# Kernel tuning notes

Hardware: AMD Instinct MI355X
Metric: run time of the kernel (lower is better)

## Reference

```python
import jax, jax.numpy as jnp
import numpy as np

BN_EPS = 1e-5


def _weight_mlp(off, Wh, bh, Wo, bo):
    # off: [Nout, k, 2] relative neighbor offsets -> [Nout, k, 9] interp coeffs
    h = jax.nn.relu(off @ Wh + bh)
    return h @ Wo + bo


def _interp_conv(x, idx, off, Wk, bk, Wh, bh, Wo, bo):
    # x: [B, Cin, Nin]; idx: [Nout, k] neighbor indices into Nin; Wk: [Cout, Cin, 9]
    a = _weight_mlp(off, Wh, bh, Wo, bo)        # [Nout, k, 9]
    feats = x[:, :, idx]                         # gather -> [B, Cin, Nout, k]
    # dynamic filter: per-neighbor kernel = a @ Wk taps, contracted with features
    y = jnp.einsum('nkt,bcnk,oct->bon', a, feats, Wk)  # [B, Cout, Nout]
    return y + bk[None, :, None]


def _bn_relu(x, g, b):
    # BatchNorm1d over [B, C, N] using batch statistics (training-mode forward)
    mean = x.mean(axis=(0, 2), keepdims=True)
    var = x.var(axis=(0, 2), keepdims=True)
    xn = (x - mean) * jax.lax.rsqrt(var + BN_EPS)
    return jax.nn.relu(xn * g[None, :, None] + b[None, :, None])


def setup_inputs() -> dict:
    key = jax.random.key(0)
    ks = jax.random.split(key, 12)
    B, N1, N2, N3, K = 8, 50176, 12544, 3136, 9
    inp = {
        'x': jax.random.normal(ks[0], (B, 3, N1), jnp.float32),
        'nbr1': jax.random.randint(ks[1], (N2, K), 0, N1, jnp.int32),
        'off1': jax.random.normal(ks[2], (N2, K, 2), jnp.float32),
        'nbr2': jax.random.randint(ks[3], (N2, K), 0, N2, jnp.int32),
        'off2': jax.random.normal(ks[4], (N2, K, 2), jnp.float32),
        'pool_idx': jax.random.randint(ks[5], (N3, K), 0, N2, jnp.int32),
        'Wh': jax.random.normal(ks[6], (2, 32), jnp.float32) * 0.5,
        'bh': jnp.zeros((32,), jnp.float32),
        'Wo': jax.random.normal(ks[7], (32, 9), jnp.float32) * 0.2,
        'bo': jnp.zeros((9,), jnp.float32),
        'W1': jax.random.normal(ks[8], (32, 3, 9), jnp.float32) * 0.2,
        'b1': jnp.zeros((32,), jnp.float32),
        'W2': jax.random.normal(ks[9], (32, 32, 9), jnp.float32) * 0.06,
        'b2': jnp.zeros((32,), jnp.float32),
        'W3': jax.random.normal(ks[10], (64, 32, 9), jnp.float32) * 0.06,
        'b3': jnp.zeros((64,), jnp.float32),
        'g1': jnp.ones((32,), jnp.float32), 'be1': jnp.zeros((32,), jnp.float32),
        'g2': jnp.ones((32,), jnp.float32), 'be2': jnp.zeros((32,), jnp.float32),
        'g3': jnp.ones((64,), jnp.float32), 'be3': jnp.zeros((64,), jnp.float32),
    }
    return inp


def reference(x, nbr1, off1, nbr2, off2, pool_idx, Wh, bh, Wo, bo,
              W1, b1, W2, b2, W3, b3, g1, be1, g2, be2, g3, be3):
    x = _bn_relu(_interp_conv(x, nbr1, off1, W1, b1, Wh, bh, Wo, bo), g1, be1)
    x = _bn_relu(_interp_conv(x, nbr2, off2, W2, b2, Wh, bh, Wo, bo), g2, be2)
    x = _bn_relu(_interp_conv(x, nbr2, off2, W3, b3, Wh, bh, Wo, bo), g3, be3)
    # MaxPoolNG: max over irregular neighbor sets from level l2 -> l3
    x = x[:, :, pool_idx].max(axis=-1)           # [B, 64, N3]
    return x
```

## Files before the change

kernel.cpp:

```cpp
#include <hip/hip_runtime.h>
#include <math.h>

#define N1C 50176
#define N2C 12544
#define N3C 3136
#define NT_TILES (N2C * 8 / 64)

typedef __attribute__((ext_vector_type(8))) short bf16x8;
typedef __attribute__((ext_vector_type(4))) float f32x4;

__device__ __forceinline__ unsigned short f2bf(float f) {
    unsigned u = __builtin_bit_cast(unsigned, f);
    u += 0x7fffu + ((u >> 16) & 1u);
    return (unsigned short)(u >> 16);
}
__device__ __forceinline__ unsigned cvtpk(float lo, float hi) {
    unsigned r;
    asm("v_cvt_pk_bf16_f32 %0, %1, %2" : "=v"(r) : "v"(lo), "v"(hi));
    return r;
}
__device__ __forceinline__ float bf2f(unsigned short u) {
    return __builtin_bit_cast(float, (unsigned)u << 16);
}
__device__ __forceinline__ float bflo(unsigned u) {
    return __builtin_bit_cast(float, u << 16);
}
__device__ __forceinline__ float bfhi(unsigned u) {
    return __builtin_bit_cast(float, u & 0xffff0000u);
}

#define TRB (N1C / 64)
#define MLB (2 * N2C * 9 / 256)
#define PWB 112

__device__ __forceinline__ void pad_one(int i, const float* __restrict__ W,
                                        unsigned short* __restrict__ Wp,
                                        int OC, int CIN, int KT) {
    int j = i & 7;
    int op = (i >> 3) & 31;
    int q = (i >> 8) & 3;
    int kt = (i >> 10) % KT;
    int g = i / (KT * 1024);
    int kp = kt * 32 + q * 8 + j;
    int t = kp / CIN, c = kp - t * CIN;
    int o = g * 32 + op;
    float v = (t < 9 && o < OC) ? W[(o * CIN + c) * 9 + t] : 0.f;
    Wp[i] = f2bf(v);
}

__global__ void prologue_kernel(const float* __restrict__ x, unsigned short* __restrict__ X0,
                                const float* __restrict__ off1, const float* __restrict__ off2,
                                const float* __restrict__ Wh, const float* __restrict__ bh,
                                const float* __restrict__ Wo, const float* __restrict__ bo,
                                float* __restrict__ A1, float* __restrict__ A2,
                                const float* __restrict__ W1, const float* __restrict__ W2,
                                const float* __restrict__ W3,
                                unsigned short* __restrict__ W1p, unsigned short* __restrict__ W2p,
                                unsigned short* __restrict__ W3p) {
    __shared__ float U[2304];
    int blk = blockIdx.x;
    int tid = threadIdx.x;
    if (blk < TRB) {
        int n0 = blk * 64;
        for (int r = tid; r < 24 * 64; r += 256) {
            int cb = r >> 6;
            int nn = r & 63;
            U[nn * 25 + cb] = x[cb * N1C + n0 + nn];
        }
        __syncthreads();
        for (int w = tid; w < 64 * 24; w += 256) {
            int nn = w / 24;
            int u = w - nn * 24;
            X0[(n0 + nn) * 24 + u] = f2bf(U[nn * 25 + u]);
        }
    } else if (blk < TRB + MLB) {
        int bi = blk - TRB;
        int idx = bi * 256 + tid;
        const float* offp;
        if (idx < N2C * 9) offp = off1 + idx * 2;
        else offp = off2 + (idx - N2C * 9) * 2;
        float o0 = offp[0], o1 = offp[1];
        float out[9];
#pragma unroll
        for (int t = 0; t < 9; t++) out[t] = bo[t];
#pragma unroll
        for (int h = 0; h < 32; h++) {
            float hv = fmaxf(o0 * Wh[h] + o1 * Wh[32 + h] + bh[h], 0.f);
#pragma unroll
            for (int t = 0; t < 9; t++) out[t] += hv * Wo[h * 9 + t];
        }
#pragma unroll
        for (int t = 0; t < 9; t++) U[tid * 9 + t] = out[t];
        __syncthreads();
        float* dst = (bi < 441) ? (A1 + (size_t)bi * 2304)
                                : (A2 + (size_t)(bi - 441) * 2304);
        for (int i = tid; i < 2304; i += 256) dst[i] = U[i];
    } else {
        int i = (blk - TRB - MLB) * 256 + tid;
        if (i < 1024) pad_one(i, W1, W1p, 32, 3, 1);
        else if (i < 10240) pad_one(i - 1024, W2, W2p, 32, 32, 9);
        else pad_one(i - 10240, W3, W3p, 64, 32, 9);
    }
}

template <int CIN, int MW, bool HAS_BN>
__global__ __launch_bounds__(256, 4)
void conv_kernel(const unsigned short* __restrict__ Xin,
                 const int* __restrict__ nbr,
                 const float* __restrict__ A,
                 const unsigned short* __restrict__ Wp,
                 const float* __restrict__ bias,
                 const float* __restrict__ bnsc,
                 const float* __restrict__ bnsh,
                 unsigned short* __restrict__ Yb,
                 double* __restrict__ Part) {
    constexpr int OC = MW * 16;
    constexpr int KREAL = 9 * CIN;
    constexpr int KROW = (KREAL + 31) & ~31;
    constexpr int KT = KROW / 32;
    constexpr int KSTR = KROW + 8;
    constexpr int PARTS = 256 / OC;
    constexpr int PCOLS = 64 / PARTS;
    constexpr int OSH = (OC == 32) ? 5 : 6;
    constexpr int YSTR = OC + 4;
    constexpr int SB1 = 64 * KSTR * 2;
    constexpr int SB2 = 64 * YSTR * 4 + PARTS * 2 * OC * 4;
    constexpr int SBYTES = SB1 > SB2 ? SB1 : SB2;
    __shared__ alignas(16) char Sraw[SBYTES];
    __shared__ float a_lds[8 * 81];
    short* S = (short*)Sraw;

    int tid = threadIdx.x;
    int tile = blockIdx.x;
    int n0 = tile * 8;

    for (int i = tid; i < 64 * KSTR; i += 256) S[i] = 0;
    for (int i = tid; i < 648; i += 256) a_lds[i] = A[(size_t)n0 * 81 + i];
    __syncthreads();
    if (tid < 192) {
        int nsub = tid / 24;
        int u = tid - nsub * 24;
        int b = u / 3, c = u - b * 3;
        int n = n0 + nsub;
        const int* nb = nbr + n * 9;
        const float* Ar = a_lds + nsub * 81;
        float s[9];
#pragma unroll
        for (int t = 0; t < 9; t++) s[t] = 0.f;
#pragma unroll
        for (int k = 0; k < 9; k++) {
            float f = bf2f(Xin[nb[k] * 24 + u]);
#pragma unroll
            for (int t = 0; t < 9; t++) s[t] = fmaf(Ar[k * 9 + t], f, s[t]);
        }
        int col = nsub * 8 + b;
#pragma unroll
        for (int t = 0; t < 9; t++) S[col * KSTR + t * 3 + c] = (short)f2bf(s[t]);
    }
    __syncthreads();

    int lane = tid & 63, wv = tid >> 6, q = lane >> 4, cl = lane & 15;
    int colg = wv * 16 + cl;

    const bf16x8* wf = (const bf16x8*)Wp;
    f32x4 acc[MW];
#pragma unroll
    for (int m = 0; m < MW; m++) acc[m] = (f32x4){0.f, 0.f, 0.f, 0.f};
#pragma unroll
    for (int kt = 0; kt < KT; kt++) {
        bf16x8 bfr = *(const bf16x8*)&S[colg * KSTR + kt * 32 + q * 8];
#pragma unroll
        for (int m = 0; m < MW; m++) {
            const bf16x8* wg = wf + (m >> 1) * (KT * 128);
            bf16x8 am = wg[(kt * 4 + q) * 32 + cl + (m & 1) * 16];
            acc[m] = __builtin_amdgcn_mfma_f32_16x16x32_bf16(am, bfr, acc[m], 0, 0, 0);
        }
    }
    __syncthreads();

    float* Yf = (float*)Sraw;
    float* P2f = Yf + 64 * YSTR;
    int C = tile * 64 + colg;
#pragma unroll
    for (int m = 0; m < MW; m++) {
        f32x4 v;
#pragma unroll
        for (int i = 0; i < 4; i++) v[i] = acc[m][i] + bias[m * 16 + q * 4 + i];
        *(f32x4*)&Yf[colg * YSTR + m * 16 + q * 4] = v;
        uint2 pk;
        pk.x = cvtpk(v[0], v[1]);
        pk.y = cvtpk(v[2], v[3]);
        *(uint2*)&Yb[(size_t)C * OC + m * 16 + q * 4] = pk;
    }
    __syncthreads();
    {
        int o = tid & (OC - 1);
        int part = tid >> OSH;
        float s = 0.f, qq = 0.f;
#pragma unroll
        for (int i = 0; i < PCOLS; i++) {
            float y = Yf[(part * PCOLS + i) * YSTR + o];
            s += y;
            qq += y * y;
        }
        P2f[part * 2 * OC + o] = s;
        P2f[part * 2 * OC + OC + o] = qq;
    }
    __syncthreads();
    if (tid < 2 * OC) {
        double v = 0.0;
#pragma unroll
        for (int p = 0; p < PARTS; p++) v += (double)P2f[p * 2 * OC + tid];
        Part[(size_t)tid * NT_TILES + tile] = v;
    }
}

template <int MW>
__global__ __launch_bounds__(256, 4)
void conv32_kernel(const unsigned short* __restrict__ Xin,
                   const int* __restrict__ nbr,
                   const float* __restrict__ A,
                   const unsigned short* __restrict__ Wp,
                   const float* __restrict__ bias,
                   const float* __restrict__ bnsc,
                   const float* __restrict__ bnsh,
                   unsigned short* __restrict__ Yb,
                   double* __restrict__ Part) {
    constexpr int OC = MW * 16;
    constexpr int KT = 9;
    constexpr int KSTR = 296;
    constexpr int PARTS = 256 / OC;
    constexpr int PCOLS = 64 / PARTS;
    constexpr int OSH = (OC == 32) ? 5 : 6;
    constexpr int YSTR = OC + 4;
    constexpr int SB1 = 64 * KSTR * 2;
    constexpr int SB2 = 64 * YSTR * 4 + PARTS * 2 * OC * 4;
    constexpr int SBYTES = SB1 > SB2 ? SB1 : SB2;
    __shared__ alignas(16) char Sraw[SBYTES];
    __shared__ float a_lds[8 * 81];
    short* S = (short*)Sraw;

    int tid = threadIdx.x;
    int wv4 = __builtin_amdgcn_readfirstlane(tid >> 6);
    int lane = tid & 63;
    int b = lane >> 3, c4 = lane & 7;
    int wv = tid >> 6, q = lane >> 4, cl = lane & 15;
    int colg = wv * 16 + cl;
    float4 scv = *(const float4*)&bnsc[4 * c4];
    float4 shv = *(const float4*)&bnsh[4 * c4];
    const uint2* Xd = (const uint2*)Xin;
    const bf16x8* wf = (const bf16x8*)Wp;
    float* Yf = (float*)Sraw;
    float* P2f = Yf + 64 * YSTR;

#pragma unroll 1
    for (int it = 0; it < 2; ++it) {
        int tile = blockIdx.x * 2 + it;
        int n0 = tile * 8;
        if (it) __syncthreads();

        uint2 fu[18];
#pragma unroll
        for (int gg = 0; gg < 2; gg++)
#pragma unroll
            for (int k = 0; k < 9; k++) {
                int j = nbr[(n0 + wv4 * 2 + gg) * 9 + k];
                fu[gg * 9 + k] = Xd[(size_t)j * 64 + lane];
            }
        for (int i = tid; i < 648; i += 256) a_lds[i] = A[(size_t)n0 * 81 + i];
        __syncthreads();
#pragma unroll
        for (int gg = 0; gg < 2; gg++) {
            const float* Ar = a_lds + (wv4 * 2 + gg) * 81;
            float s0[9], s1[9], s2[9], s3[9];
#pragma unroll
            for (int t = 0; t < 9; t++) { s0[t] = 0.f; s1[t] = 0.f; s2[t] = 0.f; s3[t] = 0.f; }
#pragma unroll
            for (int k = 0; k < 9; k++) {
                uint2 u = fu[gg * 9 + k];
                float f0 = fmaxf(fmaf(bflo(u.x), scv.x, shv.x), 0.f);
                float f1 = fmaxf(fmaf(bfhi(u.x), scv.y, shv.y), 0.f);
                float f2 = fmaxf(fmaf(bflo(u.y), scv.z, shv.z), 0.f);
                float f3 = fmaxf(fmaf(bfhi(u.y), scv.w, shv.w), 0.f);
#pragma unroll
                for (int t = 0; t < 9; t++) {
                    float a = Ar[k * 9 + t];
                    s0[t] = fmaf(a, f0, s0[t]);
                    s1[t] = fmaf(a, f1, s1[t]);
                    s2[t] = fmaf(a, f2, s2[t]);
                    s3[t] = fmaf(a, f3, s3[t]);
                }
            }
            int col = (wv4 * 2 + gg) * 8 + b;
            uint2* Srow = (uint2*)&S[col * KSTR];
#pragma unroll
            for (int t = 0; t < 9; t++) {
                uint2 pk;
                pk.x = cvtpk(s0[t], s1[t]);
                pk.y = cvtpk(s2[t], s3[t]);
                Srow[t * 8 + c4] = pk;
            }
        }
        __syncthreads();

        f32x4 acc[MW];
#pragma unroll
        for (int m = 0; m < MW; m++) acc[m] = (f32x4){0.f, 0.f, 0.f, 0.f};
#pragma unroll
        for (int kt = 0; kt < KT; kt++) {
            bf16x8 bfr = *(const bf16x8*)&S[colg * KSTR + kt * 32 + q * 8];
#pragma unroll
            for (int m = 0; m < MW; m++) {
                const bf16x8* wg = wf + (m >> 1) * (KT * 128);
                bf16x8 am = wg[(kt * 4 + q) * 32 + cl + (m & 1) * 16];
                acc[m] = __builtin_amdgcn_mfma_f32_16x16x32_bf16(am, bfr, acc[m], 0, 0, 0);
            }
        }
        __syncthreads();

        int C = tile * 64 + colg;
#pragma unroll
        for (int m = 0; m < MW; m++) {
            f32x4 v;
#pragma unroll
            for (int i = 0; i < 4; i++) v[i] = acc[m][i] + bias[m * 16 + q * 4 + i];
            *(f32x4*)&Yf[colg * YSTR + m * 16 + q * 4] = v;
            uint2 pk;
            pk.x = cvtpk(v[0], v[1]);
            pk.y = cvtpk(v[2], v[3]);
            *(uint2*)&Yb[(size_t)C * OC + m * 16 + q * 4] = pk;
        }
        __syncthreads();
        {
            int o = tid & (OC - 1);
            int part = tid >> OSH;
            float s = 0.f, qq = 0.f;
#pragma unroll
            for (int i = 0; i < PCOLS; i++) {
                float y = Yf[(part * PCOLS + i) * YSTR + o];
                s += y;
                qq += y * y;
            }
            P2f[part * 2 * OC + o] = s;
            P2f[part * 2 * OC + OC + o] = qq;
        }
        __syncthreads();
        if (tid < 2 * OC) {
            double v = 0.0;
#pragma unroll
            for (int p = 0; p < PARTS; p++) v += (double)P2f[p * 2 * OC + tid];
            Part[(size_t)tid * NT_TILES + tile] = v;
        }
    }
}

__global__ __launch_bounds__(256, 8)
void bn_reduce(const double* __restrict__ Part,
               const float* __restrict__ g, const float* __restrict__ be,
               float* __restrict__ sc, float* __restrict__ sh, int OC) {
    int o = blockIdx.x;
    int tid = threadIdx.x;
    const double* ps = Part + (size_t)o * NT_TILES;
    const double* pq = Part + (size_t)(OC + o) * NT_TILES;
    double s = 0.0, q = 0.0;
    for (int t = tid; t < NT_TILES; t += 256) {
        s += ps[t];
        q += pq[t];
    }
#pragma unroll
    for (int d = 1; d < 64; d <<= 1) {
        s += __shfl_xor(s, d);
        q += __shfl_xor(q, d);
    }
    __shared__ double red[8];
    int wv = tid >> 6;
    if ((tid & 63) == 0) { red[wv] = s; red[4 + wv] = q; }
    __syncthreads();
    if (tid == 0) {
        double S = red[0] + red[1] + red[2] + red[3];
        double Q = red[4] + red[5] + red[6] + red[7];
        double cnt = (double)N2C * 8.0;
        double mean = S / cnt;
        double var = Q / cnt - mean * mean;
        double rs = 1.0 / sqrt(var + 1e-5);
        double scale = (double)g[o] * rs;
        sc[o] = (float)scale;
        sh[o] = (float)((double)be[o] - mean * scale);
    }
}

__global__ __launch_bounds__(256, 8)
void pool_kernel(const unsigned short* __restrict__ Y3, const int* __restrict__ pidx,
                 const float* __restrict__ sc, const float* __restrict__ sh,
                 float* __restrict__ out) {
    int m0 = blockIdx.x * 2;
    int tid = threadIdx.x;
    int o2 = tid & 31;
    int b = tid >> 5;
    float s0 = sc[2 * o2], h0 = sh[2 * o2];
    float s1 = sc[2 * o2 + 1], h1 = sh[2 * o2 + 1];
    const unsigned* Y3u = (const unsigned*)Y3;
    int j0[9], j1[9];
#pragma unroll
    for (int k = 0; k < 9; k++) {
        j0[k] = pidx[m0 * 9 + k];
        j1[k] = pidx[m0 * 9 + 9 + k];
    }
    unsigned u0[9], u1[9];
#pragma unroll
    for (int k = 0; k < 9; k++) u0[k] = Y3u[(size_t)j0[k] * 256 + tid];
#pragma unroll
    for (int k = 0; k < 9; k++) u1[k] = Y3u[(size_t)j1[k] * 256 + tid];
    float a0 = 0.f, a1 = 0.f, c0 = 0.f, c1 = 0.f;
#pragma unroll
    for (int k = 0; k < 9; k++) {
        a0 = fmaxf(a0, fmaf(bflo(u0[k]), s0, h0));
        a1 = fmaxf(a1, fmaf(bfhi(u0[k]), s1, h1));
        c0 = fmaxf(c0, fmaf(bflo(u1[k]), s0, h0));
        c1 = fmaxf(c1, fmaf(bfhi(u1[k]), s1, h1));
    }
    float2 r0 = {a0, c0};
    float2 r1 = {a1, c1};
    *(float2*)(out + (size_t)(b * 64 + 2 * o2) * 3136 + m0) = r0;
    *(float2*)(out + (size_t)(b * 64 + 2 * o2 + 1) * 3136 + m0) = r1;
}

extern "C" void kernel_launch(void* const* d_in, const int* in_sizes, int n_in,
                              void* d_out, int out_size, void* d_ws, size_t ws_size,
                              hipStream_t stream) {
    const float* x    = (const float*)d_in[0];
    const int*   nbr1 = (const int*)d_in[1];
    const float* off1 = (const float*)d_in[2];
    const int*   nbr2 = (const int*)d_in[3];
    const float* off2 = (const float*)d_in[4];
    const int*   pidx = (const int*)d_in[5];
    const float* Wh   = (const float*)d_in[6];
    const float* bh   = (const float*)d_in[7];
    const float* Wo   = (const float*)d_in[8];
    const float* bo   = (const float*)d_in[9];
    const float* W1   = (const float*)d_in[10];
    const float* b1   = (const float*)d_in[11];
    const float* W2   = (const float*)d_in[12];
    const float* b2   = (const float*)d_in[13];
    const float* W3   = (const float*)d_in[14];
    const float* b3   = (const float*)d_in[15];
    const float* g1   = (const float*)d_in[16];
    const float* be1  = (const float*)d_in[17];
    const float* g2   = (const float*)d_in[18];
    const float* be2  = (const float*)d_in[19];
    const float* g3   = (const float*)d_in[20];
    const float* be3  = (const float*)d_in[21];

    char* ws = (char*)d_ws;
    size_t off = 0;
    auto alloc = [&](size_t bytes) -> void* {
        void* p = ws + off;
        off += (bytes + 255) & ~(size_t)255;
        return p;
    };
    unsigned short* X0b = (unsigned short*)alloc((size_t)N1C * 24 * 2);
    float* A1 = (float*)alloc((size_t)N2C * 81 * 4);
    float* A2 = (float*)alloc((size_t)N2C * 81 * 4);
    unsigned short* Y1b = (unsigned short*)alloc((size_t)N2C * 8 * 32 * 2);
    unsigned short* Y2b = (unsigned short*)alloc((size_t)N2C * 8 * 32 * 2);
    unsigned short* Y3b = (unsigned short*)alloc((size_t)N2C * 8 * 64 * 2);
    unsigned short* W1p = (unsigned short*)alloc(32 * 32 * 2);
    unsigned short* W2p = (unsigned short*)alloc(32 * 288 * 2);
    unsigned short* W3p = (unsigned short*)alloc(64 * 288 * 2);
    double* Part  = (double*)alloc((size_t)NT_TILES * 128 * 8);
    float*  scbuf = (float*)alloc(256 * 4);

    float* sc1 = scbuf;       float* sh1 = scbuf + 32;
    float* sc2 = scbuf + 64;  float* sh2 = scbuf + 96;
    float* sc3 = scbuf + 128; float* sh3 = scbuf + 192;

    prologue_kernel<<<TRB + MLB + PWB, 256, 0, stream>>>(
        x, X0b, off1, off2, Wh, bh, Wo, bo, A1, A2, W1, W2, W3, W1p, W2p, W3p);

    conv_kernel<3, 2, false><<<NT_TILES, 256, 0, stream>>>(
        X0b, nbr1, A1, W1p, b1, nullptr, nullptr, Y1b, Part);
    bn_reduce<<<32, 256, 0, stream>>>(Part, g1, be1, sc1, sh1, 32);

    conv32_kernel<2><<<NT_TILES / 2, 256, 0, stream>>>(
        Y1b, nbr2, A2, W2p, b2, sc1, sh1, Y2b, Part);
    bn_reduce<<<32, 256, 0, stream>>>(Part, g2, be2, sc2, sh2, 32);

    conv32_kernel<4><<<NT_TILES / 2, 256, 0, stream>>>(
        Y2b, nbr2, A2, W3p, b3, sc2, sh2, Y3b, Part);
    bn_reduce<<<64, 256, 0, stream>>>(Part, g3, be3, sc3, sh3, 64);

    pool_kernel<<<N3C / 2, 256, 0, stream>>>(Y3b, pidx, sc3, sh3, (float*)d_out);
}
```

Measured before the change: 222.9 us.

## Build MFMA B-operand in registers, dropping LDS staging in conv32 kernel

```diff
diff --git a/kernel.cpp b/kernel.cpp
--- a/kernel.cpp
+++ b/kernel.cpp
@@ -216,7 +216,7 @@
 }
 
 template <int MW>
-__global__ __launch_bounds__(256, 4)
+__global__ __launch_bounds__(256, 5)
 void conv32_kernel(const unsigned short* __restrict__ Xin,
                    const int* __restrict__ nbr,
                    const float* __restrict__ A,
@@ -227,130 +227,177 @@
                    unsigned short* __restrict__ Yb,
                    double* __restrict__ Part) {
     constexpr int OC = MW * 16;
-    constexpr int KT = 9;
-    constexpr int KSTR = 296;
     constexpr int PARTS = 256 / OC;
     constexpr int PCOLS = 64 / PARTS;
     constexpr int OSH = (OC == 32) ? 5 : 6;
     constexpr int YSTR = OC + 4;
-    constexpr int SB1 = 64 * KSTR * 2;
-    constexpr int SB2 = 64 * YSTR * 4 + PARTS * 2 * OC * 4;
-    constexpr int SBYTES = SB1 > SB2 ? SB1 : SB2;
-    __shared__ alignas(16) char Sraw[SBYTES];
-    __shared__ float a_lds[8 * 81];
-    short* S = (short*)Sraw;
+    __shared__ alignas(16) float Yf[64 * YSTR];
+    __shared__ float P2f[PARTS * 2 * OC];
+    __shared__ float a_lds[648];
 
     int tid = threadIdx.x;
-    int wv4 = __builtin_amdgcn_readfirstlane(tid >> 6);
-    int lane = tid & 63;
-    int b = lane >> 3, c4 = lane & 7;
-    int wv = tid >> 6, q = lane >> 4, cl = lane & 15;
+    int tile = blockIdx.x;
+    int n0 = tile * 8;
+    int lane = tid & 63, wv = tid >> 6;
+    int q = lane >> 4, cl = lane & 15;
+    int nl = wv * 2 + (cl >> 3);
+    int b = cl & 7;
     int colg = wv * 16 + cl;
-    float4 scv = *(const float4*)&bnsc[4 * c4];
-    float4 shv = *(const float4*)&bnsh[4 * c4];
-    const uint2* Xd = (const uint2*)Xin;
+
+    float4 sc0 = *(const float4*)&bnsc[8 * q];
+    float4 sc1 = *(const float4*)&bnsc[8 * q + 4];
+    float4 sh0 = *(const float4*)&bnsh[8 * q];
+    float4 sh1 = *(const float4*)&bnsh[8 * q + 4];
+
+    const uint4* X4 = (const uint4*)Xin;
+    uint4 fu[9];
+#pragma unroll
+    for (int k = 0; k < 9; k++) {
+        int j = nbr[(n0 + nl) * 9 + k];
+        fu[k] = X4[(size_t)(j * 8 + b) * 4 + q];
+    }
+    for (int i = tid; i < 648; i += 256) a_lds[i] = A[(size_t)n0 * 81 + i];
+    __syncthreads();
+
+    const float* Ar = a_lds + nl * 81;
     const bf16x8* wf = (const bf16x8*)Wp;
-    float* Yf = (float*)Sraw;
-    float* P2f = Yf + 64 * YSTR;
-
-#pragma unroll 1
-    for (int it = 0; it < 2; ++it) {
-        int tile = blockIdx.x * 2 + it;
-        int n0 = tile * 8;
-        if (it) __syncthreads();
-
-        uint2 fu[18];
-#pragma unroll
-        for (int gg = 0; gg < 2; gg++)
-#pragma unroll
-            for (int k = 0; k < 9; k++) {
-                int j = nbr[(n0 + wv4 * 2 + gg) * 9 + k];
-                fu[gg * 9 + k] = Xd[(size_t)j * 64 + lane];
+    f32x4 acc[MW];
+#pragma unroll
+    for (int m = 0; m < MW; m++) acc[m] = (f32x4){0.f, 0.f, 0.f, 0.f};
+
+    unsigned pk1[20];
+    {
+        float s[8][5];
+#pragma unroll
+        for (int c = 0; c < 8; c++)
+#pragma unroll
+            for (int t = 0; t < 5; t++) s[c][t] = 0.f;
+#pragma unroll
+        for (int k = 0; k < 9; k++) {
+            float f0 = fmaxf(fmaf(bflo(fu[k].x), sc0.x, sh0.x), 0.f);
+            float f1 = fmaxf(fmaf(bfhi(fu[k].x), sc0.y, sh0.y), 0.f);
+            float f2 = fmaxf(fmaf(bflo(fu[k].y), sc0.z, sh0.z), 0.f);
+            float f3 = fmaxf(fmaf(bfhi(fu[k].y), sc0.w, sh0.w), 0.f);
+            float f4 = fmaxf(fmaf(bflo(fu[k].z), sc1.x, sh1.x), 0.f);
+            float f5 = fmaxf(fmaf(bfhi(fu[k].z), sc1.y, sh1.y), 0.f);
+            float f6 = fmaxf(fmaf(bflo(fu[k].w), sc1.z, sh1.z), 0.f);
+            float f7 = fmaxf(fmaf(bfhi(fu[k].w), sc1.w, sh1.w), 0.f);
+#pragma unroll
+            for (int t = 0; t < 5; t++) {
+                float a = Ar[k * 9 + t];
+                s[0][t] = fmaf(a, f0, s[0][t]);
+                s[1][t] = fmaf(a, f1, s[1][t]);
+                s[2][t] = fmaf(a, f2, s[2][t]);
+                s[3][t] = fmaf(a, f3, s[3][t]);
+                s[4][t] = fmaf(a, f4, s[4][t]);
+                s[5][t] = fmaf(a, f5, s[5][t]);
+                s[6][t] = fmaf(a, f6, s[6][t]);
+                s[7][t] = fmaf(a, f7, s[7][t]);
             }
-        for (int i = tid; i < 648; i += 256) a_lds[i] = A[(size_t)n0 * 81 + i];
-        __syncthreads();
-#pragma unroll
-        for (int gg = 0; gg < 2; gg++) {
-            const float* Ar = a_lds + (wv4 * 2 + gg) * 81;
-            float s0[9], s1[9], s2[9], s3[9];
-#pragma unroll
-            for (int t = 0; t < 9; t++) { s0[t] = 0.f; s1[t] = 0.f; s2[t] = 0.f; s3[t] = 0.f; }
-#pragma unroll
-            for (int k = 0; k < 9; k++) {
-                uint2 u = fu[gg * 9 + k];
-                float f0 = fmaxf(fmaf(bflo(u.x), scv.x, shv.x), 0.f);
-                float f1 = fmaxf(fmaf(bfhi(u.x), scv.y, shv.y), 0.f);
-                float f2 = fmaxf(fmaf(bflo(u.y), scv.z, shv.z), 0.f);
-                float f3 = fmaxf(fmaf(bfhi(u.y), scv.w, shv.w), 0.f);
-#pragma unroll
-                for (int t = 0; t < 9; t++) {
-                    float a = Ar[k * 9 + t];
-                    s0[t] = fmaf(a, f0, s0[t]);
-                    s1[t] = fmaf(a, f1, s1[t]);
-                    s2[t] = fmaf(a, f2, s2[t]);
-                    s3[t] = fmaf(a, f3, s3[t]);
-                }
+        }
+#pragma unroll
+        for (int t = 0; t < 5; t++) {
+            pk1[t * 4 + 0] = cvtpk(s[0][t], s[1][t]);
+            pk1[t * 4 + 1] = cvtpk(s[2][t], s[3][t]);
+            pk1[t * 4 + 2] = cvtpk(s[4][t], s[5][t]);
+            pk1[t * 4 + 3] = cvtpk(s[6][t], s[7][t]);
+        }
+    }
+#pragma unroll
+    for (int kt = 0; kt < 5; kt++) {
+        uint4 uu = {pk1[kt * 4 + 0], pk1[kt * 4 + 1], pk1[kt * 4 + 2], pk1[kt * 4 + 3]};
+        bf16x8 bfr = __builtin_bit_cast(bf16x8, uu);
+#pragma unroll
+        for (int m = 0; m < MW; m++) {
+            const bf16x8* wg = wf + (m >> 1) * (9 * 128);
+            bf16x8 am = wg[(kt * 4 + q) * 32 + cl + (m & 1) * 16];
+            acc[m] = __builtin_amdgcn_mfma_f32_16x16x32_bf16(am, bfr, acc[m], 0, 0, 0);
+        }
+    }
+
+    unsigned pk2[16];
+    {
+        float s[8][4];
+#pragma unroll
+        for (int c = 0; c < 8; c++)
+#pragma unroll
+            for (int t = 0; t < 4; t++) s[c][t] = 0.f;
+#pragma unroll
+        for (int k = 0; k < 9; k++) {
+            float f0 = fmaxf(fmaf(bflo(fu[k].x), sc0.x, sh0.x), 0.f);
+            float f1 = fmaxf(fmaf(bfhi(fu[k].x), sc0.y, sh0.y), 0.f);
+            float f2 = fmaxf(fmaf(bflo(fu[k].y), sc0.z, sh0.z), 0.f);
+            float f3 = fmaxf(fmaf(bfhi(fu[k].y), sc0.w, sh0.w), 0.f);
+            float f4 = fmaxf(fmaf(bflo(fu[k].z), sc1.x, sh1.x), 0.f);
+            float f5 = fmaxf(fmaf(bfhi(fu[k].z), sc1.y, sh1.y), 0.f);
+            float f6 = fmaxf(fmaf(bflo(fu[k].w), sc1.z, sh1.z), 0.f);
+            float f7 = fmaxf(fmaf(bfhi(fu[k].w), sc1.w, sh1.w), 0.f);
+#pragma unroll
+            for (int t = 0; t < 4; t++) {
+                float a = Ar[k * 9 + 5 + t];
+                s[0][t] = fmaf(a, f0, s[0][t]);
+                s[1][t] = fmaf(a, f1, s[1][t]);
+                s[2][t] = fmaf(a, f2, s[2][t]);
+                s[3][t] = fmaf(a, f3, s[3][t]);
+                s[4][t] = fmaf(a, f4, s[4][t]);
+                s[5][t] = fmaf(a, f5, s[5][t]);
+                s[6][t] = fmaf(a, f6, s[6][t]);
+                s[7][t] = fmaf(a, f7, s[7][t]);
             }
-            int col = (wv4 * 2 + gg) * 8 + b;
-            uint2* Srow = (uint2*)&S[col * KSTR];
-#pragma unroll
-            for (int t = 0; t < 9; t++) {
-                uint2 pk;
-                pk.x = cvtpk(s0[t], s1[t]);
-                pk.y = cvtpk(s2[t], s3[t]);
-                Srow[t * 8 + c4] = pk;
-            }
-        }
-        __syncthreads();
-
-        f32x4 acc[MW];
-#pragma unroll
-        for (int m = 0; m < MW; m++) acc[m] = (f32x4){0.f, 0.f, 0.f, 0.f};
-#pragma unroll
-        for (int kt = 0; kt < KT; kt++) {
-            bf16x8 bfr = *(const bf16x8*)&S[colg * KSTR + kt * 32 + q * 8];
-#pragma unroll
-            for (int m = 0; m < MW; m++) {
-                const bf16x8* wg = wf + (m >> 1) * (KT * 128);
-                bf16x8 am = wg[(kt * 4 + q) * 32 + cl + (m & 1) * 16];
-                acc[m] = __builtin_amdgcn_mfma_f32_16x16x32_bf16(am, bfr, acc[m], 0, 0, 0);
-            }
-        }
-        __syncthreads();
-
-        int C = tile * 64 + colg;
+        }
+#pragma unroll
+        for (int t = 0; t < 4; t++) {
+            pk2[t * 4 + 0] = cvtpk(s[0][t], s[1][t]);
+            pk2[t * 4 + 1] = cvtpk(s[2][t], s[3][t]);
+            pk2[t * 4 + 2] = cvtpk(s[4][t], s[5][t]);
+            pk2[t * 4 + 3] = cvtpk(s[6][t], s[7][t]);
+        }
+    }
+#pragma unroll
+    for (int kt = 5; kt < 9; kt++) {
+        int u0 = (kt - 5) * 4;
+        uint4 uu = {pk2[u0 + 0], pk2[u0 + 1], pk2[u0 + 2], pk2[u0 + 3]};
+        bf16x8 bfr = __builtin_bit_cast(bf16x8, uu);
 #pragma unroll
         for (int m = 0; m < MW; m++) {
-            f32x4 v;
-#pragma unroll
-            for (int i = 0; i < 4; i++) v[i] = acc[m][i] + bias[m * 16 + q * 4 + i];
-            *(f32x4*)&Yf[colg * YSTR + m * 16 + q * 4] = v;
-            uint2 pk;
-            pk.x = cvtpk(v[0], v[1]);
-            pk.y = cvtpk(v[2], v[3]);
-            *(uint2*)&Yb[(size_t)C * OC + m * 16 + q * 4] = pk;
-        }
-        __syncthreads();
-        {
-            int o = tid & (OC - 1);
-            int part = tid >> OSH;
-            float s = 0.f, qq = 0.f;
-#pragma unroll
-            for (int i = 0; i < PCOLS; i++) {
-                float y = Yf[(part * PCOLS + i) * YSTR + o];
-                s += y;
-                qq += y * y;
-            }
-            P2f[part * 2 * OC + o] = s;
-            P2f[part * 2 * OC + OC + o] = qq;
-        }
-        __syncthreads();
-        if (tid < 2 * OC) {
-            double v = 0.0;
-#pragma unroll
-            for (int p = 0; p < PARTS; p++) v += (double)P2f[p * 2 * OC + tid];
-            Part[(size_t)tid * NT_TILES + tile] = v;
-        }
+            const bf16x8* wg = wf + (m >> 1) * (9 * 128);
+            bf16x8 am = wg[(kt * 4 + q) * 32 + cl + (m & 1) * 16];
+            acc[m] = __builtin_amdgcn_mfma_f32_16x16x32_bf16(am, bfr, acc[m], 0, 0, 0);
+        }
+    }
+
+    int C = tile * 64 + colg;
+#pragma unroll
+    for (int m = 0; m < MW; m++) {
+        f32x4 v;
+#pragma unroll
+        for (int i = 0; i < 4; i++) v[i] = acc[m][i] + bias[m * 16 + q * 4 + i];
+        *(f32x4*)&Yf[colg * YSTR + m * 16 + q * 4] = v;
+        uint2 pk;
+        pk.x = cvtpk(v[0], v[1]);
+        pk.y = cvtpk(v[2], v[3]);
+        *(uint2*)&Yb[(size_t)C * OC + m * 16 + q * 4] = pk;
+    }
+    __syncthreads();
+    {
+        int o = tid & (OC - 1);
+        int part = tid >> OSH;
+        float s = 0.f, qq = 0.f;
+#pragma unroll
+        for (int i = 0; i < PCOLS; i++) {
+            float y = Yf[(part * PCOLS + i) * YSTR + o];
+            s += y;
+            qq += y * y;
+        }
+        P2f[part * 2 * OC + o] = s;
+        P2f[part * 2 * OC + OC + o] = qq;
+    }
+    __syncthreads();
+    if (tid < 2 * OC) {
+        double v = 0.0;
+#pragma unroll
+        for (int p = 0; p < PARTS; p++) v += (double)P2f[p * 2 * OC + tid];
+        Part[(size_t)tid * NT_TILES + tile] = v;
     }
 }
 
@@ -481,11 +528,11 @@
         X0b, nbr1, A1, W1p, b1, nullptr, nullptr, Y1b, Part);
     bn_reduce<<<32, 256, 0, stream>>>(Part, g1, be1, sc1, sh1, 32);
 
-    conv32_kernel<2><<<NT_TILES / 2, 256, 0, stream>>>(
+    conv32_kernel<2><<<NT_TILES, 256, 0, stream>>>(
         Y1b, nbr2, A2, W2p, b2, sc1, sh1, Y2b, Part);
     bn_reduce<<<32, 256, 0, stream>>>(Part, g2, be2, sc2, sh2, 32);
 
-    conv32_kernel<4><<<NT_TILES / 2, 256, 0, stream>>>(
+    conv32_kernel<4><<<NT_TILES, 256, 0, stream>>>(
         Y2b, nbr2, A2, W3p, b3, sc2, sh2, Y3b, Part);
     bn_reduce<<<64, 256, 0, stream>>>(Part, g3, be3, sc3, sh3, 64);
 
```

Measured after the change: 302.0 us. +35.5%, slower.

## Make conv32 tile work wave-local and reduce BN stats with shuffles

Applied to the files above, without the earlier changes.

```diff
diff --git a/kernel.cpp b/kernel.cpp
--- a/kernel.cpp
+++ b/kernel.cpp
@@ -227,130 +227,119 @@
                    unsigned short* __restrict__ Yb,
                    double* __restrict__ Part) {
     constexpr int OC = MW * 16;
-    constexpr int KT = 9;
     constexpr int KSTR = 296;
-    constexpr int PARTS = 256 / OC;
-    constexpr int PCOLS = 64 / PARTS;
-    constexpr int OSH = (OC == 32) ? 5 : 6;
-    constexpr int YSTR = OC + 4;
-    constexpr int SB1 = 64 * KSTR * 2;
-    constexpr int SB2 = 64 * YSTR * 4 + PARTS * 2 * OC * 4;
-    constexpr int SBYTES = SB1 > SB2 ? SB1 : SB2;
-    __shared__ alignas(16) char Sraw[SBYTES];
-    __shared__ float a_lds[8 * 81];
-    short* S = (short*)Sraw;
+    __shared__ alignas(16) short S[64 * KSTR];
+    __shared__ float a_lds[648];
 
     int tid = threadIdx.x;
-    int wv4 = __builtin_amdgcn_readfirstlane(tid >> 6);
+    int tile = blockIdx.x;
+    int n0 = tile * 8;
+    int wv = __builtin_amdgcn_readfirstlane(tid >> 6);
     int lane = tid & 63;
     int b = lane >> 3, c4 = lane & 7;
-    int wv = tid >> 6, q = lane >> 4, cl = lane & 15;
+    int q = lane >> 4, cl = lane & 15;
     int colg = wv * 16 + cl;
+
     float4 scv = *(const float4*)&bnsc[4 * c4];
     float4 shv = *(const float4*)&bnsh[4 * c4];
     const uint2* Xd = (const uint2*)Xin;
+
+    uint2 fu[18];
+#pragma unroll
+    for (int gg = 0; gg < 2; gg++)
+#pragma unroll
+        for (int k = 0; k < 9; k++) {
+            int j = nbr[(n0 + wv * 2 + gg) * 9 + k];
+            fu[gg * 9 + k] = Xd[(size_t)j * 64 + lane];
+        }
+    {
+        int base = 162 * wv;
+        const float* Ag = A + (size_t)n0 * 81 + base;
+        a_lds[base + lane] = Ag[lane];
+        a_lds[base + 64 + lane] = Ag[64 + lane];
+        if (lane < 34) a_lds[base + 128 + lane] = Ag[128 + lane];
+    }
+
+#pragma unroll
+    for (int gg = 0; gg < 2; gg++) {
+        const float* Ar = a_lds + 162 * wv + 81 * gg;
+        float s0[9], s1[9], s2[9], s3[9];
+#pragma unroll
+        for (int t = 0; t < 9; t++) { s0[t] = 0.f; s1[t] = 0.f; s2[t] = 0.f; s3[t] = 0.f; }
+#pragma unroll
+        for (int k = 0; k < 9; k++) {
+            uint2 u = fu[gg * 9 + k];
+            float f0 = fmaxf(fmaf(bflo(u.x), scv.x, shv.x), 0.f);
+            float f1 = fmaxf(fmaf(bfhi(u.x), scv.y, shv.y), 0.f);
+            float f2 = fmaxf(fmaf(bflo(u.y), scv.z, shv.z), 0.f);
+            float f3 = fmaxf(fmaf(bfhi(u.y), scv.w, shv.w), 0.f);
+#pragma unroll
+            for (int t = 0; t < 9; t++) {
+                float a = Ar[k * 9 + t];
+                s0[t] = fmaf(a, f0, s0[t]);
+                s1[t] = fmaf(a, f1, s1[t]);
+                s2[t] = fmaf(a, f2, s2[t]);
+                s3[t] = fmaf(a, f3, s3[t]);
+            }
+        }
+        int col = (wv * 2 + gg) * 8 + b;
+        uint2* Srow = (uint2*)&S[col * KSTR];
+#pragma unroll
+        for (int t = 0; t < 9; t++) {
+            uint2 pk;
+            pk.x = cvtpk(s0[t], s1[t]);
+            pk.y = cvtpk(s2[t], s3[t]);
+            Srow[t * 8 + c4] = pk;
+        }
+    }
+
     const bf16x8* wf = (const bf16x8*)Wp;
-    float* Yf = (float*)Sraw;
-    float* P2f = Yf + 64 * YSTR;
-
-#pragma unroll 1
-    for (int it = 0; it < 2; ++it) {
-        int tile = blockIdx.x * 2 + it;
-        int n0 = tile * 8;
-        if (it) __syncthreads();
-
-        uint2 fu[18];
-#pragma unroll
-        for (int gg = 0; gg < 2; gg++)
-#pragma unroll
-            for (int k = 0; k < 9; k++) {
-                int j = nbr[(n0 + wv4 * 2 + gg) * 9 + k];
-                fu[gg * 9 + k] = Xd[(size_t)j * 64 + lane];
-            }
-        for (int i = tid; i < 648; i += 256) a_lds[i] = A[(size_t)n0 * 81 + i];
-        __syncthreads();
-#pragma unroll
-        for (int gg = 0; gg < 2; gg++) {
-            const float* Ar = a_lds + (wv4 * 2 + gg) * 81;
-            float s0[9], s1[9], s2[9], s3[9];
-#pragma unroll
-            for (int t = 0; t < 9; t++) { s0[t] = 0.f; s1[t] = 0.f; s2[t] = 0.f; s3[t] = 0.f; }
-#pragma unroll
-            for (int k = 0; k < 9; k++) {
-                uint2 u = fu[gg * 9 + k];
-                float f0 = fmaxf(fmaf(bflo(u.x), scv.x, shv.x), 0.f);
-                float f1 = fmaxf(fmaf(bfhi(u.x), scv.y, shv.y), 0.f);
-                float f2 = fmaxf(fmaf(bflo(u.y), scv.z, shv.z), 0.f);
-                float f3 = fmaxf(fmaf(bfhi(u.y), scv.w, shv.w), 0.f);
-#pragma unroll
-                for (int t = 0; t < 9; t++) {
-                    float a = Ar[k * 9 + t];
-                    s0[t] = fmaf(a, f0, s0[t]);
-                    s1[t] = fmaf(a, f1, s1[t]);
-                    s2[t] = fmaf(a, f2, s2[t]);
-                    s3[t] = fmaf(a, f3, s3[t]);
-                }
-            }
-            int col = (wv4 * 2 + gg) * 8 + b;
-            uint2* Srow = (uint2*)&S[col * KSTR];
-#pragma unroll
-            for (int t = 0; t < 9; t++) {
-                uint2 pk;
-                pk.x = cvtpk(s0[t], s1[t]);
-                pk.y = cvtpk(s2[t], s3[t]);
-                Srow[t * 8 + c4] = pk;
-            }
-        }
-        __syncthreads();
-
-        f32x4 acc[MW];
-#pragma unroll
-        for (int m = 0; m < MW; m++) acc[m] = (f32x4){0.f, 0.f, 0.f, 0.f};
-#pragma unroll
-        for (int kt = 0; kt < KT; kt++) {
-            bf16x8 bfr = *(const bf16x8*)&S[colg * KSTR + kt * 32 + q * 8];
-#pragma unroll
-            for (int m = 0; m < MW; m++) {
-                const bf16x8* wg = wf + (m >> 1) * (KT * 128);
-                bf16x8 am = wg[(kt * 4 + q) * 32 + cl + (m & 1) * 16];
-                acc[m] = __builtin_amdgcn_mfma_f32_16x16x32_bf16(am, bfr, acc[m], 0, 0, 0);
-            }
-        }
-        __syncthreads();
-
-        int C = tile * 64 + colg;
+    f32x4 acc[MW];
+#pragma unroll
+    for (int m = 0; m < MW; m++) acc[m] = (f32x4){0.f, 0.f, 0.f, 0.f};
+#pragma unroll
+    for (int kt = 0; kt < 9; kt++) {
+        bf16x8 bfr = *(const bf16x8*)&S[colg * KSTR + kt * 32 + q * 8];
 #pragma unroll
         for (int m = 0; m < MW; m++) {
-            f32x4 v;
-#pragma unroll
-            for (int i = 0; i < 4; i++) v[i] = acc[m][i] + bias[m * 16 + q * 4 + i];
-            *(f32x4*)&Yf[colg * YSTR + m * 16 + q * 4] = v;
-            uint2 pk;
-            pk.x = cvtpk(v[0], v[1]);
-            pk.y = cvtpk(v[2], v[3]);
-            *(uint2*)&Yb[(size_t)C * OC + m * 16 + q * 4] = pk;
-        }
-        __syncthreads();
-        {
-            int o = tid & (OC - 1);
-            int part = tid >> OSH;
-            float s = 0.f, qq = 0.f;
-#pragma unroll
-            for (int i = 0; i < PCOLS; i++) {
-                float y = Yf[(part * PCOLS + i) * YSTR + o];
-                s += y;
-                qq += y * y;
-            }
-            P2f[part * 2 * OC + o] = s;
-            P2f[part * 2 * OC + OC + o] = qq;
-        }
-        __syncthreads();
-        if (tid < 2 * OC) {
-            double v = 0.0;
-#pragma unroll
-            for (int p = 0; p < PARTS; p++) v += (double)P2f[p * 2 * OC + tid];
-            Part[(size_t)tid * NT_TILES + tile] = v;
-        }
+            const bf16x8* wg = wf + (m >> 1) * (9 * 128);
+            bf16x8 am = wg[(kt * 4 + q) * 32 + cl + (m & 1) * 16];
+            acc[m] = __builtin_amdgcn_mfma_f32_16x16x32_bf16(am, bfr, acc[m], 0, 0, 0);
+        }
+    }
+
+    int C = tile * 64 + colg;
+    float yv[4 * MW];
+#pragma unroll
+    for (int m = 0; m < MW; m++) {
+#pragma unroll
+        for (int i = 0; i < 4; i++) yv[m * 4 + i] = acc[m][i] + bias[m * 16 + q * 4 + i];
+        uint2 pk;
+        pk.x = cvtpk(yv[m * 4 + 0], yv[m * 4 + 1]);
+        pk.y = cvtpk(yv[m * 4 + 2], yv[m * 4 + 3]);
+        *(uint2*)&Yb[(size_t)C * OC + m * 16 + q * 4] = pk;
+    }
+    float* P2w = a_lds + 162 * wv;
+#pragma unroll
+    for (int r = 0; r < 4 * MW; r++) {
+        float ps = yv[r];
+        float pq = yv[r] * yv[r];
+#pragma unroll
+        for (int d = 1; d < 16; d <<= 1) {
+            ps += __shfl_xor(ps, d);
+            pq += __shfl_xor(pq, d);
+        }
+        if (cl == 0) {
+            int o = (r >> 2) * 16 + q * 4 + (r & 3);
+            P2w[o] = ps;
+            P2w[OC + o] = pq;
+        }
+    }
+    __syncthreads();
+    if (tid < 2 * OC) {
+        double v = (double)a_lds[tid] + (double)a_lds[162 + tid] +
+                   (double)a_lds[324 + tid] + (double)a_lds[486 + tid];
+        Part[(size_t)tid * NT_TILES + tile] = v;
     }
 }
 
@@ -481,11 +470,11 @@
         X0b, nbr1, A1, W1p, b1, nullptr, nullptr, Y1b, Part);
     bn_reduce<<<32, 256, 0, stream>>>(Part, g1, be1, sc1, sh1, 32);
 
-    conv32_kernel<2><<<NT_TILES / 2, 256, 0, stream>>>(
+    conv32_kernel<2><<<NT_TILES, 256, 0, stream>>>(
         Y1b, nbr2, A2, W2p, b2, sc1, sh1, Y2b, Part);
     bn_reduce<<<32, 256, 0, stream>>>(Part, g2, be2, sc2, sh2, 32);
 
-    conv32_kernel<4><<<NT_TILES / 2, 256, 0, stream>>>(
+    conv32_kernel<4><<<NT_TILES, 256, 0, stream>>>(
         Y2b, nbr2, A2, W3p, b3, sc2, sh2, Y3b, Part);
     bn_reduce<<<64, 256, 0, stream>>>(Part, g3, be3, sc3, sh3, 64);
 
```

Result: faster. 192.0 us (-13.9%).

## Split conv32 taps into two phases and process one tile per block

Applied to the files above, without the earlier changes.

```diff
diff --git a/kernel.cpp b/kernel.cpp
--- a/kernel.cpp
+++ b/kernel.cpp
@@ -227,130 +227,172 @@
                    unsigned short* __restrict__ Yb,
                    double* __restrict__ Part) {
     constexpr int OC = MW * 16;
-    constexpr int KT = 9;
-    constexpr int KSTR = 296;
     constexpr int PARTS = 256 / OC;
     constexpr int PCOLS = 64 / PARTS;
     constexpr int OSH = (OC == 32) ? 5 : 6;
     constexpr int YSTR = OC + 4;
-    constexpr int SB1 = 64 * KSTR * 2;
-    constexpr int SB2 = 64 * YSTR * 4 + PARTS * 2 * OC * 4;
-    constexpr int SBYTES = SB1 > SB2 ? SB1 : SB2;
-    __shared__ alignas(16) char Sraw[SBYTES];
-    __shared__ float a_lds[8 * 81];
-    short* S = (short*)Sraw;
+    constexpr int KSTR2 = 168;
+    __shared__ alignas(16) short S[64 * KSTR2];
+    __shared__ float a_lds[648];
 
     int tid = threadIdx.x;
-    int wv4 = __builtin_amdgcn_readfirstlane(tid >> 6);
+    int tile = blockIdx.x;
+    int n0 = tile * 8;
+    int wv = __builtin_amdgcn_readfirstlane(tid >> 6);
     int lane = tid & 63;
     int b = lane >> 3, c4 = lane & 7;
-    int wv = tid >> 6, q = lane >> 4, cl = lane & 15;
+    int q = lane >> 4, cl = lane & 15;
     int colg = wv * 16 + cl;
+
     float4 scv = *(const float4*)&bnsc[4 * c4];
     float4 shv = *(const float4*)&bnsh[4 * c4];
     const uint2* Xd = (const uint2*)Xin;
+
+    uint2 fu[18];
+#pragma unroll
+    for (int gg = 0; gg < 2; gg++)
+#pragma unroll
+        for (int k = 0; k < 9; k++) {
+            int j = nbr[(n0 + wv * 2 + gg) * 9 + k];
+            fu[gg * 9 + k] = Xd[(size_t)j * 64 + lane];
+        }
+    for (int i = tid; i < 648; i += 256) a_lds[i] = A[(size_t)n0 * 81 + i];
+    __syncthreads();
+
     const bf16x8* wf = (const bf16x8*)Wp;
-    float* Yf = (float*)Sraw;
+    f32x4 acc[MW];
+#pragma unroll
+    for (int m = 0; m < MW; m++) acc[m] = (f32x4){0.f, 0.f, 0.f, 0.f};
+
+#pragma unroll
+    for (int gg = 0; gg < 2; gg++) {
+        const float* Ar = a_lds + (wv * 2 + gg) * 81;
+        float s0[5], s1[5], s2[5], s3[5];
+#pragma unroll
+        for (int t = 0; t < 5; t++) { s0[t] = 0.f; s1[t] = 0.f; s2[t] = 0.f; s3[t] = 0.f; }
+#pragma unroll
+        for (int k = 0; k < 9; k++) {
+            uint2 u = fu[gg * 9 + k];
+            float f0 = fmaxf(fmaf(bflo(u.x), scv.x, shv.x), 0.f);
+            float f1 = fmaxf(fmaf(bfhi(u.x), scv.y, shv.y), 0.f);
+            float f2 = fmaxf(fmaf(bflo(u.y), scv.z, shv.z), 0.f);
+            float f3 = fmaxf(fmaf(bfhi(u.y), scv.w, shv.w), 0.f);
+#pragma unroll
+            for (int t = 0; t < 5; t++) {
+                float a = Ar[k * 9 + t];
+                s0[t] = fmaf(a, f0, s0[t]);
+                s1[t] = fmaf(a, f1, s1[t]);
+                s2[t] = fmaf(a, f2, s2[t]);
+                s3[t] = fmaf(a, f3, s3[t]);
+            }
+        }
+        int col = (wv * 2 + gg) * 8 + b;
+        uint2* Srow = (uint2*)&S[col * KSTR2];
+#pragma unroll
+        for (int t = 0; t < 5; t++) {
+            uint2 pk;
+            pk.x = cvtpk(s0[t], s1[t]);
+            pk.y = cvtpk(s2[t], s3[t]);
+            Srow[t * 8 + c4] = pk;
+        }
+    }
+#pragma unroll
+    for (int kt = 0; kt < 5; kt++) {
+        bf16x8 bfr = *(const bf16x8*)&S[colg * KSTR2 + kt * 32 + q * 8];
+#pragma unroll
+        for (int m = 0; m < MW; m++) {
+            const bf16x8* wg = wf + (m >> 1) * (9 * 128);
+            bf16x8 am = wg[(kt * 4 + q) * 32 + cl + (m & 1) * 16];
+            acc[m] = __builtin_amdgcn_mfma_f32_16x16x32_bf16(am, bfr, acc[m], 0, 0, 0);
+        }
+    }
+    __builtin_amdgcn_sched_barrier(0);
+
+#pragma unroll
+    for (int gg = 0; gg < 2; gg++)
+#pragma unroll
+        for (int k = 0; k < 9; k++) {
+            int j = nbr[(n0 + wv * 2 + gg) * 9 + k];
+            fu[gg * 9 + k] = Xd[(size_t)j * 64 + lane];
+        }
+#pragma unroll
+    for (int gg = 0; gg < 2; gg++) {
+        const float* Ar = a_lds + (wv * 2 + gg) * 81;
+        float s0[4], s1[4], s2[4], s3[4];
+#pragma unroll
+        for (int t = 0; t < 4; t++) { s0[t] = 0.f; s1[t] = 0.f; s2[t] = 0.f; s3[t] = 0.f; }
+#pragma unroll
+        for (int k = 0; k < 9; k++) {
+            uint2 u = fu[gg * 9 + k];
+            float f0 = fmaxf(fmaf(bflo(u.x), scv.x, shv.x), 0.f);
+            float f1 = fmaxf(fmaf(bfhi(u.x), scv.y, shv.y), 0.f);
+            float f2 = fmaxf(fmaf(bflo(u.y), scv.z, shv.z), 0.f);
+            float f3 = fmaxf(fmaf(bfhi(u.y), scv.w, shv.w), 0.f);
+#pragma unroll
+            for (int t = 0; t < 4; t++) {
+                float a = Ar[k * 9 + 5 + t];
+                s0[t] = fmaf(a, f0, s0[t]);
+                s1[t] = fmaf(a, f1, s1[t]);
+                s2[t] = fmaf(a, f2, s2[t]);
+                s3[t] = fmaf(a, f3, s3[t]);
+            }
+        }
+        int col = (wv * 2 + gg) * 8 + b;
+        uint2* Srow = (uint2*)&S[col * KSTR2];
+#pragma unroll
+        for (int t = 0; t < 4; t++) {
+            uint2 pk;
+            pk.x = cvtpk(s0[t], s1[t]);
+            pk.y = cvtpk(s2[t], s3[t]);
+            Srow[t * 8 + c4] = pk;
+        }
+    }
+#pragma unroll
+    for (int kt = 0; kt < 4; kt++) {
+        bf16x8 bfr = *(const bf16x8*)&S[colg * KSTR2 + kt * 32 + q * 8];
+#pragma unroll
+        for (int m = 0; m < MW; m++) {
+            const bf16x8* wg = wf + (m >> 1) * (9 * 128);
+            bf16x8 am = wg[((5 + kt) * 4 + q) * 32 + cl + (m & 1) * 16];
+            acc[m] = __builtin_amdgcn_mfma_f32_16x16x32_bf16(am, bfr, acc[m], 0, 0, 0);
+        }
+    }
+
+    __syncthreads();
+    float* Yf = (float*)S;
     float* P2f = Yf + 64 * YSTR;
-
-#pragma unroll 1
-    for (int it = 0; it < 2; ++it) {
-        int tile = blockIdx.x * 2 + it;
-        int n0 = tile * 8;
-        if (it) __syncthreads();
-
-        uint2 fu[18];
-#pragma unroll
-        for (int gg = 0; gg < 2; gg++)
-#pragma unroll
-            for (int k = 0; k < 9; k++) {
-                int j = nbr[(n0 + wv4 * 2 + gg) * 9 + k];
-                fu[gg * 9 + k] = Xd[(size_t)j * 64 + lane];
-            }
-        for (int i = tid; i < 648; i += 256) a_lds[i] = A[(size_t)n0 * 81 + i];
-        __syncthreads();
-#pragma unroll
-        for (int gg = 0; gg < 2; gg++) {
-            const float* Ar = a_lds + (wv4 * 2 + gg) * 81;
-            float s0[9], s1[9], s2[9], s3[9];
-#pragma unroll
-            for (int t = 0; t < 9; t++) { s0[t] = 0.f; s1[t] = 0.f; s2[t] = 0.f; s3[t] = 0.f; }
-#pragma unroll
-            for (int k = 0; k < 9; k++) {
-                uint2 u = fu[gg * 9 + k];
-                float f0 = fmaxf(fmaf(bflo(u.x), scv.x, shv.x), 0.f);
-                float f1 = fmaxf(fmaf(bfhi(u.x), scv.y, shv.y), 0.f);
-                float f2 = fmaxf(fmaf(bflo(u.y), scv.z, shv.z), 0.f);
-                float f3 = fmaxf(fmaf(bfhi(u.y), scv.w, shv.w), 0.f);
-#pragma unroll
-                for (int t = 0; t < 9; t++) {
-                    float a = Ar[k * 9 + t];
-                    s0[t] = fmaf(a, f0, s0[t]);
-                    s1[t] = fmaf(a, f1, s1[t]);
-                    s2[t] = fmaf(a, f2, s2[t]);
-                    s3[t] = fmaf(a, f3, s3[t]);
-                }
-            }
-            int col = (wv4 * 2 + gg) * 8 + b;
-            uint2* Srow = (uint2*)&S[col * KSTR];
-#pragma unroll
-            for (int t = 0; t < 9; t++) {
-                uint2 pk;
-                pk.x = cvtpk(s0[t], s1[t]);
-                pk.y = cvtpk(s2[t], s3[t]);
-                Srow[t * 8 + c4] = pk;
-            }
-        }
-        __syncthreads();
-
-        f32x4 acc[MW];
-#pragma unroll
-        for (int m = 0; m < MW; m++) acc[m] = (f32x4){0.f, 0.f, 0.f, 0.f};
-#pragma unroll
-        for (int kt = 0; kt < KT; kt++) {
-            bf16x8 bfr = *(const bf16x8*)&S[colg * KSTR + kt * 32 + q * 8];
-#pragma unroll
-            for (int m = 0; m < MW; m++) {
-                const bf16x8* wg = wf + (m >> 1) * (KT * 128);
-                bf16x8 am = wg[(kt * 4 + q) * 32 + cl + (m & 1) * 16];
-                acc[m] = __builtin_amdgcn_mfma_f32_16x16x32_bf16(am, bfr, acc[m], 0, 0, 0);
-            }
-        }
-        __syncthreads();
-
-        int C = tile * 64 + colg;
-#pragma unroll
-        for (int m = 0; m < MW; m++) {
-            f32x4 v;
-#pragma unroll
-            for (int i = 0; i < 4; i++) v[i] = acc[m][i] + bias[m * 16 + q * 4 + i];
-            *(f32x4*)&Yf[colg * YSTR + m * 16 + q * 4] = v;
-            uint2 pk;
-            pk.x = cvtpk(v[0], v[1]);
-            pk.y = cvtpk(v[2], v[3]);
-            *(uint2*)&Yb[(size_t)C * OC + m * 16 + q * 4] = pk;
-        }
-        __syncthreads();
-        {
-            int o = tid & (OC - 1);
-            int part = tid >> OSH;
-            float s = 0.f, qq = 0.f;
-#pragma unroll
-            for (int i = 0; i < PCOLS; i++) {
-                float y = Yf[(part * PCOLS + i) * YSTR + o];
-                s += y;
-                qq += y * y;
-            }
-            P2f[part * 2 * OC + o] = s;
-            P2f[part * 2 * OC + OC + o] = qq;
-        }
-        __syncthreads();
-        if (tid < 2 * OC) {
-            double v = 0.0;
-#pragma unroll
-            for (int p = 0; p < PARTS; p++) v += (double)P2f[p * 2 * OC + tid];
-            Part[(size_t)tid * NT_TILES + tile] = v;
-        }
+    int C = tile * 64 + colg;
+#pragma unroll
+    for (int m = 0; m < MW; m++) {
+        f32x4 v;
+#pragma unroll
+        for (int i = 0; i < 4; i++) v[i] = acc[m][i] + bias[m * 16 + q * 4 + i];
+        *(f32x4*)&Yf[colg * YSTR + m * 16 + q * 4] = v;
+        uint2 pk;
+        pk.x = cvtpk(v[0], v[1]);
+        pk.y = cvtpk(v[2], v[3]);
+        *(uint2*)&Yb[(size_t)C * OC + m * 16 + q * 4] = pk;
+    }
+    __syncthreads();
+    {
+        int o = tid & (OC - 1);
+        int part = tid >> OSH;
+        float s = 0.f, qq = 0.f;
+#pragma unroll
+        for (int i = 0; i < PCOLS; i++) {
+            float y = Yf[(part * PCOLS + i) * YSTR + o];
+            s += y;
+            qq += y * y;
+        }
+        P2f[part * 2 * OC + o] = s;
+        P2f[part * 2 * OC + OC + o] = qq;
+    }
+    __syncthreads();
+    if (tid < 2 * OC) {
+        double v = 0.0;
+#pragma unroll
+        for (int p = 0; p < PARTS; p++) v += (double)P2f[p * 2 * OC + tid];
+        Part[(size_t)tid * NT_TILES + tile] = v;
     }
 }
 
@@ -481,11 +523,11 @@
         X0b, nbr1, A1, W1p, b1, nullptr, nullptr, Y1b, Part);
     bn_reduce<<<32, 256, 0, stream>>>(Part, g1, be1, sc1, sh1, 32);
 
-    conv32_kernel<2><<<NT_TILES / 2, 256, 0, stream>>>(
+    conv32_kernel<2><<<NT_TILES, 256, 0, stream>>>(
         Y1b, nbr2, A2, W2p, b2, sc1, sh1, Y2b, Part);
     bn_reduce<<<32, 256, 0, stream>>>(Part, g2, be2, sc2, sh2, 32);
 
-    conv32_kernel<4><<<NT_TILES / 2, 256, 0, stream>>>(
+    conv32_kernel<4><<<NT_TILES, 256, 0, stream>>>(
         Y2b, nbr2, A2, W3p, b3, sc2, sh2, Y3b, Part);
     bn_reduce<<<64, 256, 0, stream>>>(Part, g3, be3, sc3, sh3, 64);
 
```

Result: faster. 190.0 us (-14.8%).
